# Optimization experiments

Hardware: AMD Instinct MI355X
Metric: run time of the kernel (lower is better)

## Reference

```python
import jax, jax.numpy as jnp
import numpy as np

N = 20000      # nodes
E = 640000     # edges (avg degree 32)
K = 4          # eigenvectors (sign-invariant batch axis)
HID = 64       # hidden_dim
EDIM = 32      # edge_dim == GINE out_channels
ODIM = 64      # out_dim of rho
EPS = 0.0      # GINEConv eps (default, not learned here)


def setup_inputs() -> dict:
    key = jax.random.key(0)
    ks = jax.random.split(key, 20)
    def g(i, shape):
        return jax.random.normal(ks[i], shape, dtype=jnp.float32) / np.float32(np.sqrt(shape[0]))
    inp = {}
    inp["x"] = jax.random.normal(ks[0], (K, N, 1), dtype=jnp.float32)
    inp["edge_attr"] = jax.random.normal(ks[1], (E, EDIM), dtype=jnp.float32)
    inp["edge_index"] = jax.random.randint(ks[2], (2, E), 0, N, dtype=jnp.int32)
    in_dims = [1, HID, HID]
    out_dims = [HID, HID, EDIM]
    i = 3
    for l in range(3):
        inp[f"l{l}_We"] = g(i, (EDIM, in_dims[l])); i += 1
        inp[f"l{l}_be"] = jnp.zeros((in_dims[l],), jnp.float32)
        inp[f"l{l}_W1"] = g(i, (in_dims[l], HID)); i += 1
        inp[f"l{l}_b1"] = jnp.zeros((HID,), jnp.float32)
        inp[f"l{l}_W2"] = g(i, (HID, out_dims[l])); i += 1
        inp[f"l{l}_b2"] = jnp.zeros((out_dims[l],), jnp.float32)
    inp["Wr1"] = g(i, (EDIM, HID)); i += 1
    inp["br1"] = jnp.zeros((HID,), jnp.float32)
    inp["Wr2"] = g(i, (HID, ODIM)); i += 1
    inp["br2"] = jnp.zeros((ODIM,), jnp.float32)
    return inp


def _gine_conv(h, src, dst, edge_attr, We, be, W1, b1, W2, b2):
    # h: [K, N, F_in]; edge linear maps edge features into node feature space
    e_emb = edge_attr @ We + be                      # [E, F_in]
    msg = jax.nn.relu(h[:, src, :] + e_emb)          # [K, E, F_in] gather
    agg = jax.vmap(lambda m: jax.ops.segment_sum(m, dst, num_segments=N))(msg)  # [K, N, F_in] scatter-add
    z = (1.0 + EPS) * h + agg
    return jax.nn.relu(z @ W1 + b1) @ W2 + b2        # per-layer MLP


def _phi(h, src, dst, edge_attr, layers):
    n = len(layers)
    for l, p in enumerate(layers):
        h = _gine_conv(h, src, dst, edge_attr, *p)
        if l < n - 1:
            h = jax.nn.relu(h)
    return h  # [K, N, EDIM]


def reference(x, edge_attr, edge_index,
              l0_We, l0_be, l0_W1, l0_b1, l0_W2, l0_b2,
              l1_We, l1_be, l1_W1, l1_b1, l1_W2, l1_b2,
              l2_We, l2_be, l2_W1, l2_b1, l2_W2, l2_b2,
              Wr1, br1, Wr2, br2):
    src = edge_index[0]
    dst = edge_index[1]
    layers = [
        (l0_We, l0_be, l0_W1, l0_b1, l0_W2, l0_b2),
        (l1_We, l1_be, l1_W1, l1_b1, l1_W2, l1_b2),
        (l2_We, l2_be, l2_W1, l2_b1, l2_W2, l2_b2),
    ]
    # sign invariance: phi(x) + phi(-x)
    phi_out = _phi(x, src, dst, edge_attr, layers) + _phi(-x, src, dst, edge_attr, layers)
    pooled = jnp.sum(phi_out, axis=0)                # sum over K eigenvectors -> [N, EDIM]
    return jax.nn.relu(pooled @ Wr1 + br1) @ Wr2 + br2  # rho MLP -> [N, ODIM]
```

## Files before the change

kernel.cpp:

```cpp
#include <hip/hip_runtime.h>

#define NN 20000
#define NE 640000
#define NCH 8
#define HID 64
#define EDIM 32
#define ODIM 64

typedef __attribute__((ext_vector_type(8))) short bf16x8;
typedef __attribute__((ext_vector_type(4))) float f32x4;

__device__ __forceinline__ float b2f(unsigned short u) {
    unsigned v = ((unsigned)u) << 16;
    return __builtin_bit_cast(float, v);
}
__device__ __forceinline__ unsigned short f2b(float f) {
    unsigned u = __builtin_bit_cast(unsigned, f);
    unsigned r = (u + 0x7fffu + ((u >> 16) & 1u)) >> 16;
    return (unsigned short)r;
}
__device__ __forceinline__ f32x4 mfma16(bf16x8 a, bf16x8 b, f32x4 c) {
    return __builtin_amdgcn_mfma_f32_16x16x32_bf16(a, b, c, 0, 0, 0);
}
__device__ __forceinline__ bf16x8 load_bfrag(const unsigned short* W, int ldn, int k0, int n0, int lane) {
    int g = lane >> 4, r = lane & 15;
    bf16x8 f;
#pragma unroll
    for (int j = 0; j < 8; ++j) f[j] = (short)W[(k0 + 8 * g + j) * ldn + n0 + r];
    return f;
}

__global__ __launch_bounds__(256) void k_prep(
    const float* We1, const float* We2, const float* W11, const float* W21,
    const float* W12, const float* W22, const float* W20, const float* Wr1,
    const float* Wr2, unsigned short* bw)
{
    int gid = blockIdx.x * 256 + threadIdx.x;
    const float* src; int off;
    if      (gid < 2048)  { src = We1; off = 0; }
    else if (gid < 4096)  { src = We2; off = 2048; }
    else if (gid < 8192)  { src = W11; off = 4096; }
    else if (gid < 12288) { src = W21; off = 8192; }
    else if (gid < 16384) { src = W12; off = 12288; }
    else if (gid < 18432) { src = W22; off = 16384; }
    else if (gid < 22528) { src = W20; off = 18432; }
    else if (gid < 24576) { src = Wr1; off = 22528; }
    else                  { src = Wr2; off = 24576; }
    bw[gid] = f2b(src[gid - off]);
}

__global__ __launch_bounds__(256) void k_hist(const int* __restrict__ ei, int* __restrict__ cnt)
{
    int e = blockIdx.x * 256 + threadIdx.x;
    if (e < NE) atomicAdd(&cnt[ei[NE + e]], 1);
}

__global__ __launch_bounds__(1024) void k_scan(const int* __restrict__ cnt,
                                               int* __restrict__ row, int* __restrict__ cursor)
{
    __shared__ int part[1024];
    int t = threadIdx.x;
    int base = t * 20;
    int s = 0;
#pragma unroll
    for (int i = 0; i < 20; ++i) { int idx = base + i; if (idx < NN) s += cnt[idx]; }
    part[t] = s;
    __syncthreads();
    int v = s;
    for (int off = 1; off < 1024; off <<= 1) {
        int add = (t >= off) ? part[t - off] : 0;
        __syncthreads();
        v += add;
        part[t] = v;
        __syncthreads();
    }
    int run = v - s;
    for (int i = 0; i < 20; ++i) {
        int idx = base + i;
        if (idx < NN) { row[idx] = run; cursor[idx] = run; run += cnt[idx]; }
    }
    if (t == 1023) row[NN] = NE;
}

__global__ __launch_bounds__(256) void k_scatter(const int* __restrict__ ei,
                                                 int* __restrict__ cursor,
                                                 int* __restrict__ srcp, int* __restrict__ eidp)
{
    int e = blockIdx.x * 256 + threadIdx.x;
    if (e < NE) {
        int d = ei[NE + e];
        int pos = atomicAdd(&cursor[d], 1);
        srcp[pos] = ei[e];
        eidp[pos] = e;
    }
}

__global__ __launch_bounds__(256) void k_permea(
    const float* __restrict__ ea, const int* __restrict__ eidp,
    const float* __restrict__ We0, const float* __restrict__ be0,
    unsigned short* __restrict__ eap, float* __restrict__ emb0)
{
    int p = blockIdx.x * 256 + threadIdx.x;
    if (p >= NE) return;
    int eid = eidp[p];
    const f32x4* s4 = (const f32x4*)(ea + (size_t)eid * 32);
    float e0 = be0[0];
#pragma unroll
    for (int h = 0; h < 4; ++h) {
        f32x4 a = s4[2 * h], b = s4[2 * h + 1];
        bf16x8 o;
#pragma unroll
        for (int j = 0; j < 4; ++j) {
            e0 = fmaf(a[j], We0[h * 8 + j], e0);
            e0 = fmaf(b[j], We0[h * 8 + 4 + j], e0);
            o[j] = (short)f2b(a[j]);
            o[4 + j] = (short)f2b(b[j]);
        }
        *(bf16x8*)(eap + (size_t)p * 32 + h * 8) = o;
    }
    emb0[p] = e0;
}

__global__ __launch_bounds__(256) void k_xt(const float* __restrict__ x, float* __restrict__ xt)
{
    int n = blockIdx.x * 256 + threadIdx.x;
    if (n < NN) {
        f32x4 v = {x[n], x[NN + n], x[2 * NN + n], x[3 * NN + n]};
        *(f32x4*)(xt + (size_t)n * 4) = v;
    }
}

__global__ __launch_bounds__(256) void k_l0_gather(
    const float* __restrict__ xt, const int* __restrict__ srcp,
    const int* __restrict__ row, const float* __restrict__ emb0,
    float* __restrict__ z0)
{
    int gwave = (blockIdx.x * 256 + threadIdx.x) >> 6;
    int half = (threadIdx.x >> 5) & 1;
    int l = threadIdx.x & 31;
    int d = gwave * 2 + half;
    if (d >= NN) return;
    int p0 = row[d], p1 = row[d + 1];
    float ap0 = 0.f, ap1 = 0.f, ap2 = 0.f, ap3 = 0.f;
    float am0 = 0.f, am1 = 0.f, am2 = 0.f, am3 = 0.f;
    for (int p = p0 + l; p < p1; p += 32) {
        float e0 = emb0[p];
        f32x4 xs = *(const f32x4*)(xt + (size_t)srcp[p] * 4);
        ap0 += fmaxf(xs[0] + e0, 0.f); am0 += fmaxf(e0 - xs[0], 0.f);
        ap1 += fmaxf(xs[1] + e0, 0.f); am1 += fmaxf(e0 - xs[1], 0.f);
        ap2 += fmaxf(xs[2] + e0, 0.f); am2 += fmaxf(e0 - xs[2], 0.f);
        ap3 += fmaxf(xs[3] + e0, 0.f); am3 += fmaxf(e0 - xs[3], 0.f);
    }
#pragma unroll
    for (int off = 1; off < 32; off <<= 1) {
        ap0 += __shfl_xor(ap0, off, 64); am0 += __shfl_xor(am0, off, 64);
        ap1 += __shfl_xor(ap1, off, 64); am1 += __shfl_xor(am1, off, 64);
        ap2 += __shfl_xor(ap2, off, 64); am2 += __shfl_xor(am2, off, 64);
        ap3 += __shfl_xor(ap3, off, 64); am3 += __shfl_xor(am3, off, 64);
    }
    if (l == 0) {
        f32x4 xd = *(const f32x4*)(xt + (size_t)d * 4);
        f32x4 zp = {xd[0] + ap0, xd[1] + ap1, xd[2] + ap2, xd[3] + ap3};
        f32x4 zm = {am0 - xd[0], am1 - xd[1], am2 - xd[2], am3 - xd[3]};
        *(f32x4*)(z0 + (size_t)d * 8) = zp;
        *(f32x4*)(z0 + (size_t)d * 8 + 4) = zm;
    }
}

__global__ __launch_bounds__(256) void k_l0_mlp(
    const float* __restrict__ z0,
    const float* __restrict__ W1, const float* __restrict__ b1,
    const unsigned short* __restrict__ W2b, const float* __restrict__ b2,
    unsigned short* __restrict__ hT)
{
    constexpr int S = 72;
    __shared__ short lds[4][16 * S];
    int lane = threadIdx.x & 63, wid = threadIdx.x >> 6, g = lane >> 4, r = lane & 15;
    short* L = lds[wid];
    bf16x8 w2f[2][4];
#pragma unroll
    for (int kk = 0; kk < 2; ++kk)
#pragma unroll
        for (int t = 0; t < 4; ++t) w2f[kk][t] = load_bfrag(W2b, 64, kk * 32, t * 16, lane);
    float b2v[4];
#pragma unroll
    for (int t = 0; t < 4; ++t) b2v[t] = b2[t * 16 + r];
    float w1a[8], w1b[8], b1a[8], b1b[8];
#pragma unroll
    for (int j = 0; j < 8; ++j) {
        w1a[j] = W1[8 * g + j];      b1a[j] = b1[8 * g + j];
        w1b[j] = W1[32 + 8 * g + j]; b1b[j] = b1[32 + 8 * g + j];
    }
    int tile = blockIdx.x * 4 + wid;
    int row0 = tile * 16;
    float zv = z0[row0 + r];
    bf16x8 a0, a1;
#pragma unroll
    for (int j = 0; j < 8; ++j) {
        a0[j] = (short)f2b(fmaxf(fmaf(zv, w1a[j], b1a[j]), 0.f));
        a1[j] = (short)f2b(fmaxf(fmaf(zv, w1b[j], b1b[j]), 0.f));
    }
    f32x4 c2[4];
#pragma unroll
    for (int t = 0; t < 4; ++t) {
        f32x4 c = {0.f, 0.f, 0.f, 0.f};
        c = mfma16(a0, w2f[0][t], c);
        c = mfma16(a1, w2f[1][t], c);
        c2[t] = c;
    }
#pragma unroll
    for (int t = 0; t < 4; ++t)
#pragma unroll
        for (int i = 0; i < 4; ++i)
            L[(4 * g + i) * S + t * 16 + r] = (short)f2b(fmaxf(c2[t][i] + b2v[t], 0.f));
    asm volatile("" ::: "memory");
    int node0 = tile * 2;
#pragma unroll
    for (int half = 0; half < 2; ++half) {
        bf16x8 v;
#pragma unroll
        for (int c = 0; c < 8; ++c) v[c] = L[(half * 8 + c) * S + lane];
        *(bf16x8*)(hT + (size_t)(node0 + half) * 512 + lane * 8) = v;
    }
}

__global__ __launch_bounds__(256) void k_gather_f(
    const int* __restrict__ srcp, const int* __restrict__ row,
    const unsigned short* __restrict__ eap,
    const unsigned short* __restrict__ Web, const float* __restrict__ be,
    const unsigned short* __restrict__ hT, unsigned short* __restrict__ z)
{
    constexpr int S4 = 66;
    __shared__ float lds[4][16 * S4];
    int lane = threadIdx.x & 63, wid = threadIdx.x >> 6, g = lane >> 4, r = lane & 15;
    float* L = lds[wid];
    bf16x8 wf[4];
#pragma unroll
    for (int t = 0; t < 4; ++t) wf[t] = load_bfrag(Web, 64, 0, t * 16, lane);
    float bev[4];
#pragma unroll
    for (int t = 0; t < 4; ++t) bev[t] = be[t * 16 + r];

    int d = blockIdx.x * 4 + wid;
    int p0 = row[d], p1 = row[d + 1];
    float acc[NCH];
#pragma unroll
    for (int c = 0; c < NCH; ++c) acc[c] = 0.f;

    for (int p = p0; p < p1; p += 16) {
        int ne = p1 - p; if (ne > 16) ne = 16;
        int pp = p + r; if (pp > p1 - 1) pp = p1 - 1;
        bf16x8 afc = *(const bf16x8*)(eap + (size_t)pp * 32 + 8 * g);
        int svc = srcp[pp];
        f32x4 c[4];
#pragma unroll
        for (int t = 0; t < 4; ++t) {
            f32x4 cc = {bev[t], bev[t], bev[t], bev[t]};
            c[t] = mfma16(afc, wf[t], cc);
        }
#pragma unroll
        for (int t = 0; t < 4; ++t)
#pragma unroll
            for (int i = 0; i < 4; ++i) {
                float v = (4 * g + i < ne) ? c[t][i] : -__builtin_inff();
                L[(4 * g + i) * S4 + t * 16 + r] = v;
            }
        asm volatile("" ::: "memory");
#pragma unroll
        for (int b = 0; b < 4; ++b) {
#pragma unroll
            for (int q = 4 * b; q < 4 * b + 4; ++q) {
                int src = __builtin_amdgcn_readlane(svc, q);
                float em = L[q * S4 + lane];
                uint4 hv = *(const uint4*)(hT + (size_t)src * 512 + (lane << 3));
                acc[0] += fmaxf(__builtin_bit_cast(float, hv.x << 16) + em, 0.f);
                acc[1] += fmaxf(__builtin_bit_cast(float, hv.x & 0xffff0000u) + em, 0.f);
                acc[2] += fmaxf(__builtin_bit_cast(float, hv.y << 16) + em, 0.f);
                acc[3] += fmaxf(__builtin_bit_cast(float, hv.y & 0xffff0000u) + em, 0.f);
                acc[4] += fmaxf(__builtin_bit_cast(float, hv.z << 16) + em, 0.f);
                acc[5] += fmaxf(__builtin_bit_cast(float, hv.z & 0xffff0000u) + em, 0.f);
                acc[6] += fmaxf(__builtin_bit_cast(float, hv.w << 16) + em, 0.f);
                acc[7] += fmaxf(__builtin_bit_cast(float, hv.w & 0xffff0000u) + em, 0.f);
            }
            __builtin_amdgcn_sched_barrier(0);
        }
        asm volatile("" ::: "memory");
    }

    uint4 hd = *(const uint4*)(hT + (size_t)d * 512 + (lane << 3));
    unsigned hw[4] = {hd.x, hd.y, hd.z, hd.w};
    unsigned short* zd = z + (size_t)d * 8 * 64 + lane;
#pragma unroll
    for (int j = 0; j < 4; ++j) {
        float lo = __builtin_bit_cast(float, hw[j] << 16);
        float hi = __builtin_bit_cast(float, hw[j] & 0xffff0000u);
        zd[(2 * j) * 64] = f2b(lo + acc[2 * j]);
        zd[(2 * j + 1) * 64] = f2b(hi + acc[2 * j + 1]);
    }
}

template <int OUT, bool RELU2, bool TOHT>
__global__ __launch_bounds__(256) void k_mlp(
    const unsigned short* __restrict__ z,
    const unsigned short* __restrict__ W1b, const float* __restrict__ b1,
    const unsigned short* __restrict__ W2b, const float* __restrict__ b2,
    unsigned short* __restrict__ hout)
{
    constexpr int S1 = 72;
    constexpr int S2 = (OUT == 64) ? 72 : 40;
    constexpr int NT2 = OUT / 16;
    __shared__ short lds[4][16 * S1];
    int lane = threadIdx.x & 63, wid = threadIdx.x >> 6, g = lane >> 4, r = lane & 15;
    short* L = lds[wid];

    bf16x8 w1f[2][4];
#pragma unroll
    for (int kk = 0; kk < 2; ++kk)
#pragma unroll
        for (int t = 0; t < 4; ++t) w1f[kk][t] = load_bfrag(W1b, 64, kk * 32, t * 16, lane);
    bf16x8 w2f[2][NT2];
#pragma unroll
    for (int kk = 0; kk < 2; ++kk)
#pragma unroll
        for (int t = 0; t < NT2; ++t) w2f[kk][t] = load_bfrag(W2b, OUT, kk * 32, t * 16, lane);
    float b1v[4], b2v[NT2];
#pragma unroll
    for (int t = 0; t < 4; ++t) b1v[t] = b1[t * 16 + r];
#pragma unroll
    for (int t = 0; t < NT2; ++t) b2v[t] = b2[t * 16 + r];

    int tile = blockIdx.x * 4 + wid;
    int row0 = tile * 16;

    bf16x8 a0 = *(const bf16x8*)(z + (size_t)(row0 + r) * 64 + 8 * g);
    bf16x8 a1 = *(const bf16x8*)(z + (size_t)(row0 + r) * 64 + 32 + 8 * g);
    f32x4 c1[4];
#pragma unroll
    for (int t = 0; t < 4; ++t) {
        f32x4 c = {0.f, 0.f, 0.f, 0.f};
        c = mfma16(a0, w1f[0][t], c);
        c = mfma16(a1, w1f[1][t], c);
        c1[t] = c;
    }
#pragma unroll
    for (int t = 0; t < 4; ++t)
#pragma unroll
        for (int i = 0; i < 4; ++i)
            L[(4 * g + i) * S1 + t * 16 + r] = (short)f2b(fmaxf(c1[t][i] + b1v[t], 0.f));
    asm volatile("" ::: "memory");
    bf16x8 t0 = *(const bf16x8*)(L + r * S1 + 8 * g);
    bf16x8 t1 = *(const bf16x8*)(L + r * S1 + 32 + 8 * g);
    f32x4 c2[NT2];
#pragma unroll
    for (int t = 0; t < NT2; ++t) {
        f32x4 c = {0.f, 0.f, 0.f, 0.f};
        c = mfma16(t0, w2f[0][t], c);
        c = mfma16(t1, w2f[1][t], c);
        c2[t] = c;
    }
    asm volatile("" ::: "memory");
#pragma unroll
    for (int t = 0; t < NT2; ++t)
#pragma unroll
        for (int i = 0; i < 4; ++i) {
            float v = c2[t][i] + b2v[t];
            if (RELU2) v = fmaxf(v, 0.f);
            L[(4 * g + i) * S2 + t * 16 + r] = (short)f2b(v);
        }
    asm volatile("" ::: "memory");
    if (TOHT) {
        int node0 = tile * 2;
#pragma unroll
        for (int half = 0; half < 2; ++half) {
            bf16x8 v;
#pragma unroll
            for (int c = 0; c < 8; ++c) v[c] = L[(half * 8 + c) * S2 + lane];
            *(bf16x8*)(hout + (size_t)(node0 + half) * 512 + lane * 8) = v;
        }
    } else {
        bf16x8 o0 = *(const bf16x8*)(L + r * S2 + 8 * g);
        *(bf16x8*)(hout + (size_t)(row0 + r) * OUT + 8 * g) = o0;
    }
}

__global__ __launch_bounds__(256) void k_rho(
    const unsigned short* __restrict__ h2,
    const unsigned short* __restrict__ Wr1b, const float* __restrict__ br1,
    const unsigned short* __restrict__ Wr2b, const float* __restrict__ br2,
    float* __restrict__ out)
{
    constexpr int S = 72;
    __shared__ short lds[4][16 * S];
    int lane = threadIdx.x & 63, wid = threadIdx.x >> 6, g = lane >> 4, r = lane & 15;
    short* L = lds[wid];
    int tile = blockIdx.x * 4 + wid;
    if (tile * 16 >= NN) return;
    bf16x8 w1f[4], w2f[2][4];
#pragma unroll
    for (int t = 0; t < 4; ++t) w1f[t] = load_bfrag(Wr1b, 64, 0, t * 16, lane);
#pragma unroll
    for (int kk = 0; kk < 2; ++kk)
#pragma unroll
        for (int t = 0; t < 4; ++t) w2f[kk][t] = load_bfrag(Wr2b, 64, kk * 32, t * 16, lane);
    float b1v[4], b2v[4];
#pragma unroll
    for (int t = 0; t < 4; ++t) { b1v[t] = br1[t * 16 + r]; b2v[t] = br2[t * 16 + r]; }

    int n = tile * 16 + r;
    float s[8] = {0.f, 0.f, 0.f, 0.f, 0.f, 0.f, 0.f, 0.f};
#pragma unroll
    for (int c = 0; c < NCH; ++c) {
        bf16x8 hv = *(const bf16x8*)(h2 + ((size_t)n * 8 + c) * 32 + 8 * g);
#pragma unroll
        for (int j = 0; j < 8; ++j) s[j] += b2f((unsigned short)hv[j]);
    }
    bf16x8 af;
#pragma unroll
    for (int j = 0; j < 8; ++j) af[j] = (short)f2b(s[j]);
    f32x4 c1[4];
#pragma unroll
    for (int t = 0; t < 4; ++t) {
        f32x4 c = {0.f, 0.f, 0.f, 0.f};
        c1[t] = mfma16(af, w1f[t], c);
    }
#pragma unroll
    for (int t = 0; t < 4; ++t)
#pragma unroll
        for (int i = 0; i < 4; ++i)
            L[(4 * g + i) * S + t * 16 + r] = (short)f2b(fmaxf(c1[t][i] + b1v[t], 0.f));
    asm volatile("" ::: "memory");
    bf16x8 t0 = *(const bf16x8*)(L + r * S + 8 * g);
    bf16x8 t1 = *(const bf16x8*)(L + r * S + 32 + 8 * g);
    f32x4 c2[4];
#pragma unroll
    for (int t = 0; t < 4; ++t) {
        f32x4 c = {0.f, 0.f, 0.f, 0.f};
        c = mfma16(t0, w2f[0][t], c);
        c = mfma16(t1, w2f[1][t], c);
        c2[t] = c;
    }
    int nb = tile * 16;
#pragma unroll
    for (int t = 0; t < 4; ++t)
#pragma unroll
        for (int i = 0; i < 4; ++i)
            out[(size_t)(nb + 4 * g + i) * 64 + t * 16 + r] = c2[t][i] + b2v[t];
}

extern "C" void kernel_launch(void* const* d_in, const int* in_sizes, int n_in,
                              void* d_out, int out_size, void* d_ws, size_t ws_size,
                              hipStream_t stream)
{
    const float* x   = (const float*)d_in[0];
    const float* ea  = (const float*)d_in[1];
    const int*   ei  = (const int*)d_in[2];
    const float* We0 = (const float*)d_in[3];
    const float* be0 = (const float*)d_in[4];
    const float* W10 = (const float*)d_in[5];
    const float* b10 = (const float*)d_in[6];
    const float* W20 = (const float*)d_in[7];
    const float* b20 = (const float*)d_in[8];
    const float* We1 = (const float*)d_in[9];
    const float* be1 = (const float*)d_in[10];
    const float* W11 = (const float*)d_in[11];
    const float* b11 = (const float*)d_in[12];
    const float* W21 = (const float*)d_in[13];
    const float* b21 = (const float*)d_in[14];
    const float* We2 = (const float*)d_in[15];
    const float* be2 = (const float*)d_in[16];
    const float* W12 = (const float*)d_in[17];
    const float* b12 = (const float*)d_in[18];
    const float* W22 = (const float*)d_in[19];
    const float* b22 = (const float*)d_in[20];
    const float* Wr1 = (const float*)d_in[21];
    const float* br1 = (const float*)d_in[22];
    const float* Wr2 = (const float*)d_in[23];
    const float* br2 = (const float*)d_in[24];
    float* out = (float*)d_out;

    char* base = (char*)d_ws;
    unsigned short* hT   = (unsigned short*)base; base += (size_t)NN * 512 * 2;
    unsigned short* z    = (unsigned short*)base; base += (size_t)160000 * 64 * 2;
    unsigned short* h2   = (unsigned short*)base; base += (size_t)160000 * 32 * 2;
    unsigned short* eap  = (unsigned short*)base; base += (size_t)NE * 32 * 2;
    float* emb0          = (float*)base;          base += (size_t)NE * 4;
    float* z0            = (float*)base;          base += (size_t)160000 * 4;
    float* xt            = (float*)base;          base += (size_t)NN * 4 * 4;
    int* srcp            = (int*)base;            base += (size_t)NE * 4;
    int* eidp            = (int*)base;            base += (size_t)NE * 4;
    int* row             = (int*)base;            base += 80128;
    int* cnt             = (int*)base;            base += 80128;
    int* cursor          = (int*)base;            base += 80128;
    unsigned short* bw   = (unsigned short*)base;

    const unsigned short* bWe1 = bw;
    const unsigned short* bWe2 = bw + 2048;
    const unsigned short* bW11 = bw + 4096;
    const unsigned short* bW21 = bw + 8192;
    const unsigned short* bW12 = bw + 12288;
    const unsigned short* bW22 = bw + 16384;
    const unsigned short* bW20 = bw + 18432;
    const unsigned short* bWr1 = bw + 22528;
    const unsigned short* bWr2 = bw + 24576;

    k_prep<<<112, 256, 0, stream>>>(We1, We2, W11, W21, W12, W22, W20, Wr1, Wr2, bw);
    hipMemsetAsync(cnt, 0, NN * sizeof(int), stream);
    k_hist<<<NE / 256, 256, 0, stream>>>(ei, cnt);
    k_scan<<<1, 1024, 0, stream>>>(cnt, row, cursor);
    k_scatter<<<NE / 256, 256, 0, stream>>>(ei, cursor, srcp, eidp);
    k_permea<<<NE / 256, 256, 0, stream>>>(ea, eidp, We0, be0, eap, emb0);
    k_xt<<<(NN + 255) / 256, 256, 0, stream>>>(x, xt);

    k_l0_gather<<<(NN / 2 + 3) / 4, 256, 0, stream>>>(xt, srcp, row, emb0, z0);
    k_l0_mlp<<<2500, 256, 0, stream>>>(z0, W10, b10, bW20, b20, hT);

    k_gather_f<<<NN / 4, 256, 0, stream>>>(srcp, row, eap, bWe1, be1, hT, z);
    k_mlp<64, true, true><<<2500, 256, 0, stream>>>(z, bW11, b11, bW21, b21, hT);

    k_gather_f<<<NN / 4, 256, 0, stream>>>(srcp, row, eap, bWe2, be2, hT, z);
    k_mlp<32, false, false><<<2500, 256, 0, stream>>>(z, bW12, b12, bW22, b22, h2);

    k_rho<<<313, 256, 0, stream>>>(h2, bWr1, br1, bWr2, br2, out);
}
```

Baseline: 382.1 us.

## Fuse gather with per-layer MLP and merge CSR preprocessing kernels

Each layer's gather-aggregate kernel now runs the two-layer MLP itself. The block's 4 nodes (32 rows, each node holding 8 channel rows) are staged through shared memory and split across the 4 waves for the MFMA matmuls, which removes the round trip of the z buffer through global memory and one launch per layer. The scatter and edge-attribute permute kernels are merged so edges are written straight to their CSR slot without the eidp indirection, and the x transpose is folded into the histogram kernel. Layer 1 writes to a second hT buffer, since other blocks still read hT while it runs. The costs are extra block-level syncs and shared-memory staging inside the gather kernel, and reading edge attributes in edge order while writing them scattered.

New measurement: 392.1 us. 2.6% more time.

```diff
diff --git a/kernel.cpp b/kernel.cpp
--- a/kernel.cpp
+++ b/kernel.cpp
@@ -49,10 +49,15 @@
     bw[gid] = f2b(src[gid - off]);
 }
 
-__global__ __launch_bounds__(256) void k_hist(const int* __restrict__ ei, int* __restrict__ cnt)
+__global__ __launch_bounds__(256) void k_hist(const int* __restrict__ ei, int* __restrict__ cnt,
+                                              const float* __restrict__ x, float* __restrict__ xt)
 {
     int e = blockIdx.x * 256 + threadIdx.x;
     if (e < NE) atomicAdd(&cnt[ei[NE + e]], 1);
+    if (e < NN) {
+        f32x4 v = {x[e], x[NN + e], x[2 * NN + e], x[3 * NN + e]};
+        *(f32x4*)(xt + (size_t)e * 4) = v;
+    }
 }
 
 __global__ __launch_bounds__(1024) void k_scan(const int* __restrict__ cnt,
@@ -82,28 +87,17 @@
     if (t == 1023) row[NN] = NE;
 }
 
-__global__ __launch_bounds__(256) void k_scatter(const int* __restrict__ ei,
-                                                 int* __restrict__ cursor,
-                                                 int* __restrict__ srcp, int* __restrict__ eidp)
+__global__ __launch_bounds__(256) void k_scatter2(
+    const int* __restrict__ ei, int* __restrict__ cursor,
+    const float* __restrict__ ea, const float* __restrict__ We0, const float* __restrict__ be0,
+    int* __restrict__ srcp, unsigned short* __restrict__ eap, float* __restrict__ emb0)
 {
     int e = blockIdx.x * 256 + threadIdx.x;
-    if (e < NE) {
-        int d = ei[NE + e];
-        int pos = atomicAdd(&cursor[d], 1);
-        srcp[pos] = ei[e];
-        eidp[pos] = e;
-    }
-}
-
-__global__ __launch_bounds__(256) void k_permea(
-    const float* __restrict__ ea, const int* __restrict__ eidp,
-    const float* __restrict__ We0, const float* __restrict__ be0,
-    unsigned short* __restrict__ eap, float* __restrict__ emb0)
-{
-    int p = blockIdx.x * 256 + threadIdx.x;
-    if (p >= NE) return;
-    int eid = eidp[p];
-    const f32x4* s4 = (const f32x4*)(ea + (size_t)eid * 32);
+    if (e >= NE) return;
+    int d = ei[NE + e];
+    int pos = atomicAdd(&cursor[d], 1);
+    srcp[pos] = ei[e];
+    const f32x4* s4 = (const f32x4*)(ea + (size_t)e * 32);
     float e0 = be0[0];
 #pragma unroll
     for (int h = 0; h < 4; ++h) {
@@ -116,18 +110,9 @@
             o[j] = (short)f2b(a[j]);
             o[4 + j] = (short)f2b(b[j]);
         }
-        *(bf16x8*)(eap + (size_t)p * 32 + h * 8) = o;
-    }
-    emb0[p] = e0;
-}
-
-__global__ __launch_bounds__(256) void k_xt(const float* __restrict__ x, float* __restrict__ xt)
-{
-    int n = blockIdx.x * 256 + threadIdx.x;
-    if (n < NN) {
-        f32x4 v = {x[n], x[NN + n], x[2 * NN + n], x[3 * NN + n]};
-        *(f32x4*)(xt + (size_t)n * 4) = v;
-    }
+        *(bf16x8*)(eap + (size_t)pos * 32 + h * 8) = o;
+    }
+    emb0[pos] = e0;
 }
 
 __global__ __launch_bounds__(256) void k_l0_gather(
@@ -224,16 +209,23 @@
     }
 }
 
-__global__ __launch_bounds__(256) void k_gather_f(
+template <int OUT>
+__global__ __launch_bounds__(256) void k_gather_mlp(
     const int* __restrict__ srcp, const int* __restrict__ row,
     const unsigned short* __restrict__ eap,
     const unsigned short* __restrict__ Web, const float* __restrict__ be,
-    const unsigned short* __restrict__ hT, unsigned short* __restrict__ z)
+    const unsigned short* __restrict__ W1b, const float* __restrict__ b1,
+    const unsigned short* __restrict__ W2b, const float* __restrict__ b2,
+    const unsigned short* __restrict__ hin, unsigned short* __restrict__ hout)
 {
     constexpr int S4 = 66;
-    __shared__ float lds[4][16 * S4];
+    constexpr int SZ = 80;
+    __shared__ float smem[4 * 16 * S4];
     int lane = threadIdx.x & 63, wid = threadIdx.x >> 6, g = lane >> 4, r = lane & 15;
-    float* L = lds[wid];
+    float* L = smem + wid * 16 * S4;
+    short* Lz = (short*)smem;
+    short* Lt = Lz + 32 * SZ;
+
     bf16x8 wf[4];
 #pragma unroll
     for (int t = 0; t < 4; ++t) wf[t] = load_bfrag(Web, 64, 0, t * 16, lane);
@@ -272,7 +264,7 @@
             for (int q = 4 * b; q < 4 * b + 4; ++q) {
                 int src = __builtin_amdgcn_readlane(svc, q);
                 float em = L[q * S4 + lane];
-                uint4 hv = *(const uint4*)(hT + (size_t)src * 512 + (lane << 3));
+                uint4 hv = *(const uint4*)(hin + (size_t)src * 512 + (lane << 3));
                 acc[0] += fmaxf(__builtin_bit_cast(float, hv.x << 16) + em, 0.f);
                 acc[1] += fmaxf(__builtin_bit_cast(float, hv.x & 0xffff0000u) + em, 0.f);
                 acc[2] += fmaxf(__builtin_bit_cast(float, hv.y << 16) + em, 0.f);
@@ -287,99 +279,78 @@
         asm volatile("" ::: "memory");
     }
 
-    uint4 hd = *(const uint4*)(hT + (size_t)d * 512 + (lane << 3));
-    unsigned hw[4] = {hd.x, hd.y, hd.z, hd.w};
-    unsigned short* zd = z + (size_t)d * 8 * 64 + lane;
-#pragma unroll
-    for (int j = 0; j < 4; ++j) {
-        float lo = __builtin_bit_cast(float, hw[j] << 16);
-        float hi = __builtin_bit_cast(float, hw[j] & 0xffff0000u);
-        zd[(2 * j) * 64] = f2b(lo + acc[2 * j]);
-        zd[(2 * j + 1) * 64] = f2b(hi + acc[2 * j + 1]);
-    }
-}
-
-template <int OUT, bool RELU2, bool TOHT>
-__global__ __launch_bounds__(256) void k_mlp(
-    const unsigned short* __restrict__ z,
-    const unsigned short* __restrict__ W1b, const float* __restrict__ b1,
-    const unsigned short* __restrict__ W2b, const float* __restrict__ b2,
-    unsigned short* __restrict__ hout)
-{
-    constexpr int S1 = 72;
-    constexpr int S2 = (OUT == 64) ? 72 : 40;
-    constexpr int NT2 = OUT / 16;
-    __shared__ short lds[4][16 * S1];
-    int lane = threadIdx.x & 63, wid = threadIdx.x >> 6, g = lane >> 4, r = lane & 15;
-    short* L = lds[wid];
-
-    bf16x8 w1f[2][4];
+    uint4 hd = *(const uint4*)(hin + (size_t)d * 512 + (lane << 3));
+    float zval[8];
+    {
+        unsigned hw[4] = {hd.x, hd.y, hd.z, hd.w};
+#pragma unroll
+        for (int j = 0; j < 4; ++j) {
+            zval[2 * j]     = __builtin_bit_cast(float, hw[j] << 16) + acc[2 * j];
+            zval[2 * j + 1] = __builtin_bit_cast(float, hw[j] & 0xffff0000u) + acc[2 * j + 1];
+        }
+    }
+
+    __syncthreads();
+#pragma unroll
+    for (int c = 0; c < 8; ++c)
+        Lz[(wid * 8 + c) * SZ + lane] = (short)f2b(zval[c]);
+    __syncthreads();
+
+    int t = wid >> 1;
+    int nh = wid & 1;
+    bf16x8 w1f[2][2];
 #pragma unroll
     for (int kk = 0; kk < 2; ++kk)
 #pragma unroll
-        for (int t = 0; t < 4; ++t) w1f[kk][t] = load_bfrag(W1b, 64, kk * 32, t * 16, lane);
-    bf16x8 w2f[2][NT2];
-#pragma unroll
-    for (int kk = 0; kk < 2; ++kk)
-#pragma unroll
-        for (int t = 0; t < NT2; ++t) w2f[kk][t] = load_bfrag(W2b, OUT, kk * 32, t * 16, lane);
-    float b1v[4], b2v[NT2];
-#pragma unroll
-    for (int t = 0; t < 4; ++t) b1v[t] = b1[t * 16 + r];
-#pragma unroll
-    for (int t = 0; t < NT2; ++t) b2v[t] = b2[t * 16 + r];
-
-    int tile = blockIdx.x * 4 + wid;
-    int row0 = tile * 16;
-
-    bf16x8 a0 = *(const bf16x8*)(z + (size_t)(row0 + r) * 64 + 8 * g);
-    bf16x8 a1 = *(const bf16x8*)(z + (size_t)(row0 + r) * 64 + 32 + 8 * g);
-    f32x4 c1[4];
-#pragma unroll
-    for (int t = 0; t < 4; ++t) {
-        f32x4 c = {0.f, 0.f, 0.f, 0.f};
-        c = mfma16(a0, w1f[0][t], c);
-        c = mfma16(a1, w1f[1][t], c);
-        c1[t] = c;
-    }
-#pragma unroll
-    for (int t = 0; t < 4; ++t)
+        for (int nt = 0; nt < 2; ++nt)
+            w1f[kk][nt] = load_bfrag(W1b, 64, kk * 32, nh * 32 + nt * 16, lane);
+    bf16x8 a0 = *(const bf16x8*)(Lz + (t * 16 + r) * SZ + 8 * g);
+    bf16x8 a1 = *(const bf16x8*)(Lz + (t * 16 + r) * SZ + 32 + 8 * g);
+#pragma unroll
+    for (int nt = 0; nt < 2; ++nt) {
+        float bb = b1[nh * 32 + nt * 16 + r];
+        f32x4 cc = {bb, bb, bb, bb};
+        cc = mfma16(a0, w1f[0][nt], cc);
+        cc = mfma16(a1, w1f[1][nt], cc);
 #pragma unroll
         for (int i = 0; i < 4; ++i)
-            L[(4 * g + i) * S1 + t * 16 + r] = (short)f2b(fmaxf(c1[t][i] + b1v[t], 0.f));
-    asm volatile("" ::: "memory");
-    bf16x8 t0 = *(const bf16x8*)(L + r * S1 + 8 * g);
-    bf16x8 t1 = *(const bf16x8*)(L + r * S1 + 32 + 8 * g);
-    f32x4 c2[NT2];
-#pragma unroll
-    for (int t = 0; t < NT2; ++t) {
-        f32x4 c = {0.f, 0.f, 0.f, 0.f};
-        c = mfma16(t0, w2f[0][t], c);
-        c = mfma16(t1, w2f[1][t], c);
-        c2[t] = c;
-    }
-    asm volatile("" ::: "memory");
-#pragma unroll
-    for (int t = 0; t < NT2; ++t)
-#pragma unroll
-        for (int i = 0; i < 4; ++i) {
-            float v = c2[t][i] + b2v[t];
-            if (RELU2) v = fmaxf(v, 0.f);
-            L[(4 * g + i) * S2 + t * 16 + r] = (short)f2b(v);
+            Lt[(t * 16 + 4 * g + i) * SZ + nh * 32 + nt * 16 + r] = (short)f2b(fmaxf(cc[i], 0.f));
+    }
+    __syncthreads();
+
+    bf16x8 t0 = *(const bf16x8*)(Lt + (t * 16 + r) * SZ + 8 * g);
+    bf16x8 t1 = *(const bf16x8*)(Lt + (t * 16 + r) * SZ + 32 + 8 * g);
+    if (OUT == 64) {
+#pragma unroll
+        for (int nt = 0; nt < 2; ++nt) {
+            float bb = b2[nh * 32 + nt * 16 + r];
+            f32x4 cc = {bb, bb, bb, bb};
+            cc = mfma16(t0, load_bfrag(W2b, 64, 0, nh * 32 + nt * 16, lane), cc);
+            cc = mfma16(t1, load_bfrag(W2b, 64, 32, nh * 32 + nt * 16, lane), cc);
+#pragma unroll
+            for (int i = 0; i < 4; ++i)
+                Lz[(t * 16 + 4 * g + i) * SZ + nh * 32 + nt * 16 + r] = (short)f2b(fmaxf(cc[i], 0.f));
         }
-    asm volatile("" ::: "memory");
-    if (TOHT) {
-        int node0 = tile * 2;
-#pragma unroll
-        for (int half = 0; half < 2; ++half) {
-            bf16x8 v;
-#pragma unroll
-            for (int c = 0; c < 8; ++c) v[c] = L[(half * 8 + c) * S2 + lane];
-            *(bf16x8*)(hout + (size_t)(node0 + half) * 512 + lane * 8) = v;
-        }
+        __syncthreads();
+        bf16x8 v;
+#pragma unroll
+        for (int c = 0; c < 8; ++c) v[c] = Lz[(wid * 8 + c) * SZ + lane];
+        *(bf16x8*)(hout + (size_t)d * 512 + lane * 8) = v;
     } else {
-        bf16x8 o0 = *(const bf16x8*)(L + r * S2 + 8 * g);
-        *(bf16x8*)(hout + (size_t)(row0 + r) * OUT + 8 * g) = o0;
+        float bb = b2[nh * 16 + r];
+        f32x4 cc = {bb, bb, bb, bb};
+        cc = mfma16(t0, load_bfrag(W2b, 32, 0, nh * 16, lane), cc);
+        cc = mfma16(t1, load_bfrag(W2b, 32, 32, nh * 16, lane), cc);
+#pragma unroll
+        for (int i = 0; i < 4; ++i)
+            Lz[(t * 16 + 4 * g + i) * SZ + nh * 16 + r] = (short)f2b(cc[i]);
+        __syncthreads();
+        int r8 = lane >> 3;
+        int cg = (lane & 7) * 4;
+        short o[4];
+#pragma unroll
+        for (int j = 0; j < 4; ++j) o[j] = Lz[(wid * 8 + r8) * SZ + cg + j];
+        *(short4*)(hout + ((size_t)d * 8 + r8) * 32 + cg) = make_short4(o[0], o[1], o[2], o[3]);
     }
 }
 
@@ -480,14 +451,13 @@
 
     char* base = (char*)d_ws;
     unsigned short* hT   = (unsigned short*)base; base += (size_t)NN * 512 * 2;
-    unsigned short* z    = (unsigned short*)base; base += (size_t)160000 * 64 * 2;
+    unsigned short* hT2  = (unsigned short*)base; base += (size_t)NN * 512 * 2;
     unsigned short* h2   = (unsigned short*)base; base += (size_t)160000 * 32 * 2;
     unsigned short* eap  = (unsigned short*)base; base += (size_t)NE * 32 * 2;
     float* emb0          = (float*)base;          base += (size_t)NE * 4;
     float* z0            = (float*)base;          base += (size_t)160000 * 4;
     float* xt            = (float*)base;          base += (size_t)NN * 4 * 4;
     int* srcp            = (int*)base;            base += (size_t)NE * 4;
-    int* eidp            = (int*)base;            base += (size_t)NE * 4;
     int* row             = (int*)base;            base += 80128;
     int* cnt             = (int*)base;            base += 80128;
     int* cursor          = (int*)base;            base += 80128;
@@ -505,20 +475,18 @@
 
     k_prep<<<112, 256, 0, stream>>>(We1, We2, W11, W21, W12, W22, W20, Wr1, Wr2, bw);
     hipMemsetAsync(cnt, 0, NN * sizeof(int), stream);
-    k_hist<<<NE / 256, 256, 0, stream>>>(ei, cnt);
+    k_hist<<<NE / 256, 256, 0, stream>>>(ei, cnt, x, xt);
     k_scan<<<1, 1024, 0, stream>>>(cnt, row, cursor);
-    k_scatter<<<NE / 256, 256, 0, stream>>>(ei, cursor, srcp, eidp);
-    k_permea<<<NE / 256, 256, 0, stream>>>(ea, eidp, We0, be0, eap, emb0);
-    k_xt<<<(NN + 255) / 256, 256, 0, stream>>>(x, xt);
+    k_scatter2<<<NE / 256, 256, 0, stream>>>(ei, cursor, ea, We0, be0, srcp, eap, emb0);
 
     k_l0_gather<<<(NN / 2 + 3) / 4, 256, 0, stream>>>(xt, srcp, row, emb0, z0);
     k_l0_mlp<<<2500, 256, 0, stream>>>(z0, W10, b10, bW20, b20, hT);
 
-    k_gather_f<<<NN / 4, 256, 0, stream>>>(srcp, row, eap, bWe1, be1, hT, z);
-    k_mlp<64, true, true><<<2500, 256, 0, stream>>>(z, bW11, b11, bW21, b21, hT);
-
-    k_gather_f<<<NN / 4, 256, 0, stream>>>(srcp, row, eap, bWe2, be2, hT, z);
-    k_mlp<32, false, false><<<2500, 256, 0, stream>>>(z, bW12, b12, bW22, b22, h2);
+    k_gather_mlp<64><<<NN / 4, 256, 0, stream>>>(srcp, row, eap, bWe1, be1,
+                                                 bW11, b11, bW21, b21, hT, hT2);
+
+    k_gather_mlp<32><<<NN / 4, 256, 0, stream>>>(srcp, row, eap, bWe2, be2,
+                                                 bW12, b12, bW22, b22, hT2, h2);
 
     k_rho<<<313, 256, 0, stream>>>(h2, bWr1, br1, bWr2, br2, out);
 }
```

## Fuse CSR scatter with edge-attr permute, fold transpose into histogram, bf16 LDS in gather

Applied to the files above, without the earlier changes.

Merges k_scatter and k_permea into a single kernel that reads edge attributes in original order and writes the bf16 copy and layer-0 edge embedding directly to the CSR position. This drops the eidp array and a kernel launch, and the edge-attribute reads become coalesced while the writes become scattered. The x transpose moves into k_hist, removing another launch. k_gather_f now keeps the edge-weight fragments in shared memory instead of registers and stores the edge embeddings as bf16, which halves LDS traffic and register pressure but adds rounding to the messages.

Measured after the change: 358.1 us. 1.07x faster.

```diff
diff --git a/kernel.cpp b/kernel.cpp
--- a/kernel.cpp
+++ b/kernel.cpp
@@ -49,10 +49,15 @@
     bw[gid] = f2b(src[gid - off]);
 }
 
-__global__ __launch_bounds__(256) void k_hist(const int* __restrict__ ei, int* __restrict__ cnt)
+__global__ __launch_bounds__(256) void k_hist(const int* __restrict__ ei, int* __restrict__ cnt,
+                                              const float* __restrict__ x, float* __restrict__ xt)
 {
     int e = blockIdx.x * 256 + threadIdx.x;
     if (e < NE) atomicAdd(&cnt[ei[NE + e]], 1);
+    if (e < NN) {
+        f32x4 v = {x[e], x[NN + e], x[2 * NN + e], x[3 * NN + e]};
+        *(f32x4*)(xt + (size_t)e * 4) = v;
+    }
 }
 
 __global__ __launch_bounds__(1024) void k_scan(const int* __restrict__ cnt,
@@ -82,28 +87,17 @@
     if (t == 1023) row[NN] = NE;
 }
 
-__global__ __launch_bounds__(256) void k_scatter(const int* __restrict__ ei,
-                                                 int* __restrict__ cursor,
-                                                 int* __restrict__ srcp, int* __restrict__ eidp)
+__global__ __launch_bounds__(256) void k_scatter2(
+    const int* __restrict__ ei, int* __restrict__ cursor,
+    const float* __restrict__ ea, const float* __restrict__ We0, const float* __restrict__ be0,
+    int* __restrict__ srcp, unsigned short* __restrict__ eap, float* __restrict__ emb0)
 {
     int e = blockIdx.x * 256 + threadIdx.x;
-    if (e < NE) {
-        int d = ei[NE + e];
-        int pos = atomicAdd(&cursor[d], 1);
-        srcp[pos] = ei[e];
-        eidp[pos] = e;
-    }
-}
-
-__global__ __launch_bounds__(256) void k_permea(
-    const float* __restrict__ ea, const int* __restrict__ eidp,
-    const float* __restrict__ We0, const float* __restrict__ be0,
-    unsigned short* __restrict__ eap, float* __restrict__ emb0)
-{
-    int p = blockIdx.x * 256 + threadIdx.x;
-    if (p >= NE) return;
-    int eid = eidp[p];
-    const f32x4* s4 = (const f32x4*)(ea + (size_t)eid * 32);
+    if (e >= NE) return;
+    int d = ei[NE + e];
+    int pos = atomicAdd(&cursor[d], 1);
+    srcp[pos] = ei[e];
+    const f32x4* s4 = (const f32x4*)(ea + (size_t)e * 32);
     float e0 = be0[0];
 #pragma unroll
     for (int h = 0; h < 4; ++h) {
@@ -116,18 +110,9 @@
             o[j] = (short)f2b(a[j]);
             o[4 + j] = (short)f2b(b[j]);
         }
-        *(bf16x8*)(eap + (size_t)p * 32 + h * 8) = o;
-    }
-    emb0[p] = e0;
-}
-
-__global__ __launch_bounds__(256) void k_xt(const float* __restrict__ x, float* __restrict__ xt)
-{
-    int n = blockIdx.x * 256 + threadIdx.x;
-    if (n < NN) {
-        f32x4 v = {x[n], x[NN + n], x[2 * NN + n], x[3 * NN + n]};
-        *(f32x4*)(xt + (size_t)n * 4) = v;
-    }
+        *(bf16x8*)(eap + (size_t)pos * 32 + h * 8) = o;
+    }
+    emb0[pos] = e0;
 }
 
 __global__ __launch_bounds__(256) void k_l0_gather(
@@ -230,16 +215,20 @@
     const unsigned short* __restrict__ Web, const float* __restrict__ be,
     const unsigned short* __restrict__ hT, unsigned short* __restrict__ z)
 {
-    constexpr int S4 = 66;
-    __shared__ float lds[4][16 * S4];
+    constexpr int SE = 66;
+    __shared__ short Lw[4 * 64 * 8];
+    __shared__ short Lem[4][16 * SE];
     int lane = threadIdx.x & 63, wid = threadIdx.x >> 6, g = lane >> 4, r = lane & 15;
-    float* L = lds[wid];
-    bf16x8 wf[4];
-#pragma unroll
-    for (int t = 0; t < 4; ++t) wf[t] = load_bfrag(Web, 64, 0, t * 16, lane);
+    short* Le = Lem[wid];
+
+    {
+        bf16x8 f = load_bfrag(Web, 64, 0, wid * 16, lane);
+        *(bf16x8*)(Lw + (wid * 64 + lane) * 8) = f;
+    }
     float bev[4];
 #pragma unroll
     for (int t = 0; t < 4; ++t) bev[t] = be[t * 16 + r];
+    __syncthreads();
 
     int d = blockIdx.x * 4 + wid;
     int p0 = row[d], p1 = row[d + 1];
@@ -252,26 +241,24 @@
         int pp = p + r; if (pp > p1 - 1) pp = p1 - 1;
         bf16x8 afc = *(const bf16x8*)(eap + (size_t)pp * 32 + 8 * g);
         int svc = srcp[pp];
-        f32x4 c[4];
 #pragma unroll
         for (int t = 0; t < 4; ++t) {
+            bf16x8 wfrag = *(const bf16x8*)(Lw + (t * 64 + lane) * 8);
             f32x4 cc = {bev[t], bev[t], bev[t], bev[t]};
-            c[t] = mfma16(afc, wf[t], cc);
+            cc = mfma16(afc, wfrag, cc);
+#pragma unroll
+            for (int i = 0; i < 4; ++i) {
+                unsigned short v = (4 * g + i < ne) ? f2b(cc[i]) : (unsigned short)0xFF80;
+                Le[(4 * g + i) * SE + t * 16 + r] = (short)v;
+            }
         }
-#pragma unroll
-        for (int t = 0; t < 4; ++t)
-#pragma unroll
-            for (int i = 0; i < 4; ++i) {
-                float v = (4 * g + i < ne) ? c[t][i] : -__builtin_inff();
-                L[(4 * g + i) * S4 + t * 16 + r] = v;
-            }
         asm volatile("" ::: "memory");
 #pragma unroll
         for (int b = 0; b < 4; ++b) {
 #pragma unroll
             for (int q = 4 * b; q < 4 * b + 4; ++q) {
                 int src = __builtin_amdgcn_readlane(svc, q);
-                float em = L[q * S4 + lane];
+                float em = b2f((unsigned short)Le[q * SE + lane]);
                 uint4 hv = *(const uint4*)(hT + (size_t)src * 512 + (lane << 3));
                 acc[0] += fmaxf(__builtin_bit_cast(float, hv.x << 16) + em, 0.f);
                 acc[1] += fmaxf(__builtin_bit_cast(float, hv.x & 0xffff0000u) + em, 0.f);
@@ -487,7 +474,6 @@
     float* z0            = (float*)base;          base += (size_t)160000 * 4;
     float* xt            = (float*)base;          base += (size_t)NN * 4 * 4;
     int* srcp            = (int*)base;            base += (size_t)NE * 4;
-    int* eidp            = (int*)base;            base += (size_t)NE * 4;
     int* row             = (int*)base;            base += 80128;
     int* cnt             = (int*)base;            base += 80128;
     int* cursor          = (int*)base;            base += 80128;
@@ -505,11 +491,9 @@
 
     k_prep<<<112, 256, 0, stream>>>(We1, We2, W11, W21, W12, W22, W20, Wr1, Wr2, bw);
     hipMemsetAsync(cnt, 0, NN * sizeof(int), stream);
-    k_hist<<<NE / 256, 256, 0, stream>>>(ei, cnt);
+    k_hist<<<NE / 256, 256, 0, stream>>>(ei, cnt, x, xt);
     k_scan<<<1, 1024, 0, stream>>>(cnt, row, cursor);
-    k_scatter<<<NE / 256, 256, 0, stream>>>(ei, cursor, srcp, eidp);
-    k_permea<<<NE / 256, 256, 0, stream>>>(ea, eidp, We0, be0, eap, emb0);
-    k_xt<<<(NN + 255) / 256, 256, 0, stream>>>(x, xt);
+    k_scatter2<<<NE / 256, 256, 0, stream>>>(ei, cursor, ea, We0, be0, srcp, eap, emb0);
 
     k_l0_gather<<<(NN / 2 + 3) / 4, 256, 0, stream>>>(xt, srcp, row, emb0, z0);
     k_l0_mlp<<<2500, 256, 0, stream>>>(z0, W10, b10, bW20, b20, hT);
```
